# Kernel optimization log

Measured on AMD Instinct MI355X. Metric: run time of the kernel, lower is better.

Reference implementation:

```python
import jax, jax.numpy as jnp
import numpy as np
from math import log2

B, N, H, DH, BSZ = 4, 4096, 16, 64, 16
DIM = H * DH
EPS = 1e-8


def setup_inputs() -> dict:
    key = jax.random.key(0)
    ks = jax.random.split(key, 7)
    s = 0.02
    return {
        "hidden_states": jax.random.normal(ks[0], (B, N, DIM), jnp.float32),
        "Wq": jax.random.normal(ks[1], (DIM, DIM), jnp.float32) * s,
        "bq": jax.random.normal(ks[2], (DIM,), jnp.float32) * s,
        "Wk": jax.random.normal(ks[3], (DIM, DIM), jnp.float32) * s,
        "bk": jax.random.normal(ks[4], (DIM,), jnp.float32) * s,
        "Wv": jax.random.normal(ks[5], (DIM, DIM), jnp.float32) * s,
        "bv": jax.random.normal(ks[6], (DIM,), jnp.float32) * s,
    }


def _hattention(q, k, v):
    # q, k, v: [(b*h), n, dh]; n is a power of two divisible by BSZ
    bh, n, dh = q.shape
    num_levels = int(log2(n // BSZ)) - 2  # coarsen until 4 blocks remain

    # coarsening: mean-pool q and k, sum-pool v (mask=None path)
    qkvs = [(q, k, v)]
    for _ in range(num_levels):
        q = q.reshape(bh, -1, 2, dh).mean(axis=2)
        k = k.reshape(bh, -1, 2, dh).mean(axis=2)
        v = v.reshape(bh, -1, 2, dh).sum(axis=2)
        qkvs.append((q, k, v))

    def flip_blocks(t):
        # swap adjacent blocks to capture off-diagonal interactions
        nb = t.shape[1]
        return t.reshape(bh, nb // 2, 2, BSZ, dh)[:, :, ::-1].reshape(bh, nb, BSZ, dh)

    Ys = []
    L = len(qkvs)
    for ind in range(L):
        qq, kk, vv = qkvs[L - 1 - ind]  # reversed: coarsest first
        is_last = ind == L - 1          # finest level: pure block-diagonal
        blk = lambda t: t.reshape(bh, -1, BSZ, dh)
        qq, kk, vv = blk(qq), blk(kk), blk(vv)
        if not is_last:
            kk = flip_blocks(kk)
            vv = flip_blocks(vv)
        S = jnp.einsum('bnid,bnjd->bnij', qq, kk)
        S = S - jnp.max(S, axis=-1, keepdims=True)
        A = jnp.exp(S)  # unnormalized attention weights
        y = jnp.einsum('bnij,bnjd->bnid', A, vv)
        Ys.append((y.reshape(bh, -1, dh), A.sum(axis=-1).reshape(bh, -1)))

    # interpolate: upsample coarse numerators/denominators and accumulate
    Y, A = Ys[0]
    for Y_l, A_l in Ys[1:]:
        Y = jnp.repeat(Y, 2, axis=1) + Y_l
        A = jnp.repeat(A, 2, axis=1) + A_l
    return Y / (A + EPS)[..., None]


def reference(hidden_states, Wq, bq, Wk, bk, Wv, bv):
    b, n, d = hidden_states.shape
    q = hidden_states @ Wq + bq
    k = hidden_states @ Wk + bk
    v = hidden_states @ Wv + bv
    split_heads = lambda t: t.reshape(b, n, H, DH).transpose(0, 2, 1, 3).reshape(b * H, n, DH)
    q, k, v = split_heads(q), split_heads(k), split_heads(v)
    q = q * (DH ** -0.5)
    out = _hattention(q, k, v)  # [(b*h), n, dh]
    return out.reshape(b, H, n, DH).transpose(0, 2, 1, 3).reshape(b, n, H * DH)
```

## Files before the change

kernel.cpp:

```cpp
#include <hip/hip_runtime.h>
#include <hip/hip_bf16.h>

typedef unsigned short u16;
typedef unsigned int u32;
typedef __bf16 bf16x8 __attribute__((ext_vector_type(8)));
typedef float f32x4 __attribute__((ext_vector_type(4)));
typedef u16 u16x4 __attribute__((ext_vector_type(4)));
typedef u16 u16x8 __attribute__((ext_vector_type(8)));

#define N_    4096
#define H_    16
#define BH_   64
#define DIM_  1024
#define MTOK  16384

#define RB1 262144
#define RB2 393216
#define RB3 458752
#define RB4 491520
#define RB5 507904
#define RB6 516096

__device__ __forceinline__ float bf2f(u16 u) {
  union { u32 i; float f; } x; x.i = ((u32)u) << 16; return x.f;
}
__device__ __forceinline__ u16 f2bf(float f) {
  union { float f; u32 i; } x; x.f = f;
  u32 r = x.i + 0x7fffu + ((x.i >> 16) & 1u);
  return (u16)(r >> 16);
}

__device__ __forceinline__ void gload_lds16(const u16* g, u16* l) {
  __builtin_amdgcn_global_load_lds(
      (const __attribute__((address_space(1))) void*)g,
      (__attribute__((address_space(3))) void*)l, 16, 0, 0);
}

__global__ __launch_bounds__(256) void k_hid2bf(const float* __restrict__ in,
                                                u16* __restrict__ out, int n4) {
  int i = blockIdx.x * 256 + threadIdx.x;
  if (i >= n4) return;
  f32x4 v = reinterpret_cast<const f32x4*>(in)[i];
  u16x4 o;
  o[0] = f2bf(v[0]); o[1] = f2bf(v[1]); o[2] = f2bf(v[2]); o[3] = f2bf(v[3]);
  reinterpret_cast<u16x4*>(out)[i] = o;
}

__global__ __launch_bounds__(256) void k_transpose(const float* __restrict__ Wq,
                                                   const float* __restrict__ Wk,
                                                   const float* __restrict__ Wv,
                                                   u16* __restrict__ Wt) {
  __shared__ float tile[32][33];
  const float* W = (blockIdx.z == 0) ? Wq : ((blockIdx.z == 1) ? Wk : Wv);
  int n0 = blockIdx.x * 32, k0 = blockIdx.y * 32;
  int tx = threadIdx.x, ty = threadIdx.y;
  #pragma unroll
  for (int r = ty; r < 32; r += 8)
    tile[r][tx] = W[(size_t)(k0 + r) * DIM_ + n0 + tx];
  __syncthreads();
  u16* o = Wt + (size_t)blockIdx.z * DIM_ * DIM_;
  #pragma unroll
  for (int r = ty; r < 32; r += 8)
    o[(size_t)(n0 + r) * DIM_ + k0 + tx] = f2bf(tile[tx][r]);
}

__global__ __launch_bounds__(256) void k_qkv_gemm(
    const u16* __restrict__ hid,
    const u16* __restrict__ Wt,
    const float* __restrict__ bq, const float* __restrict__ bk, const float* __restrict__ bv,
    u16* __restrict__ qout, u16* __restrict__ kout, u16* __restrict__ vout) {
  const int wsel = blockIdx.z;
  const int m0 = blockIdx.x * 128;
  const int n0 = blockIdx.y * 128;
  __shared__ u16 As[128 * 64];
  __shared__ u16 Bs[128 * 64];
  const int t = threadIdx.x;
  const int lane = t & 63, wave = t >> 6;
  const int wm = (wave >> 1) * 64, wn = (wave & 1) * 64;
  f32x4 acc[4][4];
  #pragma unroll
  for (int m = 0; m < 4; m++)
    #pragma unroll
    for (int n = 0; n < 4; n++) acc[m][n] = (f32x4){0.f, 0.f, 0.f, 0.f};

  const int srow = t >> 3;
  const int sslot = (t & 7) ^ (srow & 7);
  const u16* Ag = hid + ((size_t)m0 + srow) * DIM_ + sslot * 8;
  const u16* Bg = Wt + (size_t)wsel * DIM_ * DIM_ + ((size_t)n0 + srow) * DIM_ + sslot * 8;
  u16* AsT = &As[t * 8];
  u16* BsT = &Bs[t * 8];
  const int lr = lane & 15, kg = lane >> 4;

  for (int k0 = 0; k0 < DIM_; k0 += 64) {
    #pragma unroll
    for (int j = 0; j < 4; j++) {
      gload_lds16(Ag + k0 + j * (32 * DIM_), AsT + j * 2048);
      gload_lds16(Bg + k0 + j * (32 * DIM_), BsT + j * 2048);
    }
    __syncthreads();
    #pragma unroll
    for (int ks = 0; ks < 2; ks++) {
      bf16x8 af[4], bfr[4];
      const int sw = ((ks * 4 + kg) ^ (lr & 7)) * 8;
      #pragma unroll
      for (int m = 0; m < 4; m++)
        af[m] = *reinterpret_cast<const bf16x8*>(&As[(wm + m * 16 + lr) * 64 + sw]);
      #pragma unroll
      for (int n = 0; n < 4; n++)
        bfr[n] = *reinterpret_cast<const bf16x8*>(&Bs[(wn + n * 16 + lr) * 64 + sw]);
      #pragma unroll
      for (int m = 0; m < 4; m++)
        #pragma unroll
        for (int n = 0; n < 4; n++)
          acc[m][n] = __builtin_amdgcn_mfma_f32_16x16x32_bf16(af[m], bfr[n], acc[m][n], 0, 0, 0);
    }
    __syncthreads();
  }

  const float* bias = (wsel == 0) ? bq : ((wsel == 1) ? bk : bv);
  u16* dst = (wsel == 0) ? qout : ((wsel == 1) ? kout : vout);
  const float scale = (wsel == 0) ? 0.125f : 1.0f;
  const bool isv = (wsel == 2);
  const float s1 = isv ? 1.f : 0.5f, s2 = isv ? 1.f : 0.25f;
  const float s3 = isv ? 1.f : 0.125f, s4 = isv ? 1.f : 0.0625f;
  const int rg = lane >> 4;
  const int b = m0 >> 12;
  const int posb = m0 & (N_ - 1);
  const int h = (n0 + wn) >> 6;
  const size_t bh = (size_t)(b * H_ + h);

  #pragma unroll
  for (int m = 0; m < 4; m++) {
    const int plm = wm + m * 16;
    #pragma unroll
    for (int n = 0; n < 4; n++) {
      const int d = n * 16 + lr;
      const float bias_v = bias[n0 + wn + d];
      float v0 = (acc[m][n][0] + bias_v) * scale;
      float v1 = (acc[m][n][1] + bias_v) * scale;
      float v2 = (acc[m][n][2] + bias_v) * scale;
      float v3 = (acc[m][n][3] + bias_v) * scale;
      const int pl = plm + rg * 4;
      size_t r0 = (bh * N_ + posb + pl) * 64 + d;
      dst[r0] = f2bf(v0); dst[r0 + 64] = f2bf(v1);
      dst[r0 + 128] = f2bf(v2); dst[r0 + 192] = f2bf(v3);
      float c1a = v0 + v1, c1b = v2 + v3;
      size_t r1 = ((size_t)RB1 + bh * 2048 + (size_t)((posb + pl) >> 1)) * 64 + d;
      dst[r1] = f2bf(c1a * s1);
      dst[r1 + 64] = f2bf(c1b * s1);
      float c2 = c1a + c1b;
      dst[((size_t)RB2 + bh * 1024 + (size_t)((posb + pl) >> 2)) * 64 + d] = f2bf(c2 * s2);
      float c3 = c2 + __shfl_xor(c2, 16);
      float c4 = c3 + __shfl_xor(c3, 32);
      if ((rg & 1) == 0)
        dst[((size_t)RB3 + bh * 512 + (size_t)(((posb + plm) >> 3) + (rg >> 1))) * 64 + d] =
            f2bf(c3 * s3);
      if (rg == 0)
        dst[((size_t)RB4 + bh * 256 + (size_t)((posb + plm) >> 4)) * 64 + d] = f2bf(c4 * s4);
    }
  }
}

__global__ __launch_bounds__(256) void k_coarsen56(u16* __restrict__ qb, u16* __restrict__ kb,
                                                   u16* __restrict__ vb) {
  int t = blockIdx.x * 256 + threadIdx.x;
  int dg = t & 7;
  int p6 = (t >> 3) & 63;
  int bh = (t >> 9) & 63;
  int z = t >> 15;
  u16* buf = (z == 0) ? qb : ((z == 1) ? kb : vb);
  const bool isv = (z == 2);
  const float s5 = isv ? 1.f : 0.5f, s6 = isv ? 1.f : 0.25f;
  const u16* src = buf + ((size_t)RB4 + bh * 256 + p6 * 4) * 64 + dg * 8;
  float a5[8], a6[8];
  #pragma unroll
  for (int e = 0; e < 8; e++) { a5[e] = 0.f; a6[e] = 0.f; }
  #pragma unroll
  for (int i = 0; i < 4; i++) {
    u16x8 x = *reinterpret_cast<const u16x8*>(src + (size_t)i * 64);
    #pragma unroll
    for (int e = 0; e < 8; e++) a5[e] += bf2f(x[e]);
    if ((i & 1) == 1) {
      u16x8 o;
      #pragma unroll
      for (int e = 0; e < 8; e++) { o[e] = f2bf(a5[e] * s5); a6[e] += a5[e]; a5[e] = 0.f; }
      *reinterpret_cast<u16x8*>(buf + ((size_t)RB5 + bh * 128 + p6 * 2 + (i >> 1)) * 64 + dg * 8) = o;
    }
  }
  u16x8 o;
  #pragma unroll
  for (int e = 0; e < 8; e++) o[e] = f2bf(a6[e] * s6);
  *reinterpret_cast<u16x8*>(buf + ((size_t)RB6 + bh * 64 + p6) * 64 + dg * 8) = o;
}

__device__ __forceinline__ void qk_softmax(const u16* __restrict__ qb_, size_t qrow,
                                           const u16* __restrict__ kb_, size_t kvrow,
                                           int lane, f32x4& p, float& asum) {
  const int lr = lane & 15, g = lane >> 4;
  const u16* kp = kb_ + (kvrow + lr) * 64 + g * 8;
  const u16* qp = qb_ + (qrow + lr) * 64 + g * 8;
  bf16x8 ka0 = *reinterpret_cast<const bf16x8*>(kp);
  bf16x8 ka1 = *reinterpret_cast<const bf16x8*>(kp + 32);
  bf16x8 qa0 = *reinterpret_cast<const bf16x8*>(qp);
  bf16x8 qa1 = *reinterpret_cast<const bf16x8*>(qp + 32);
  f32x4 s = (f32x4){0.f, 0.f, 0.f, 0.f};
  s = __builtin_amdgcn_mfma_f32_16x16x32_bf16(ka0, qa0, s, 0, 0, 0);
  s = __builtin_amdgcn_mfma_f32_16x16x32_bf16(ka1, qa1, s, 0, 0, 0);
  float mx = fmaxf(fmaxf(s[0], s[1]), fmaxf(s[2], s[3]));
  mx = fmaxf(mx, __shfl_xor(mx, 16));
  mx = fmaxf(mx, __shfl_xor(mx, 32));
  #pragma unroll
  for (int i = 0; i < 4; i++) p[i] = __expf(s[i] - mx);
  asum = p[0] + p[1] + p[2] + p[3];
  asum += __shfl_xor(asum, 16);
  asum += __shfl_xor(asum, 32);
}

__device__ __forceinline__ bf16x8 prep_pb(const f32x4& p, int lane) {
  const int g = lane >> 4;
  const int src = (lane & 15) + ((g & 1) << 5);
  float tl[4], th[4];
  #pragma unroll
  for (int i = 0; i < 4; i++) {
    tl[i] = __shfl(p[i], src);
    th[i] = __shfl(p[i], src + 16);
  }
  const bool act = (g < 2);
  union { u16 u[8]; bf16x8 b; } cvt;
  #pragma unroll
  for (int i = 0; i < 4; i++) {
    cvt.u[i] = act ? f2bf(tl[i]) : (u16)0;
    cvt.u[4 + i] = act ? f2bf(th[i]) : (u16)0;
  }
  return cvt.b;
}

__device__ __forceinline__ f32x4 pv_chunk(const u16* __restrict__ vb_, size_t kvrow,
                                          int c, int lane, bf16x8 pb) {
  const int lr = lane & 15, g = lane >> 4;
  const u16* vp = vb_ + (kvrow + (size_t)(g & 1) * 8) * 64 + c * 16 + lr;
  union { u16 u[8]; bf16x8 b; } va;
  #pragma unroll
  for (int e = 0; e < 8; e++) va.u[e] = vp[(size_t)e * 64];
  f32x4 y = (f32x4){0.f, 0.f, 0.f, 0.f};
  return __builtin_amdgcn_mfma_f32_16x16x32_bf16(va.b, pb, y, 0, 0, 0);
}

__global__ __launch_bounds__(256) void k_attn_rest(
    const u16* __restrict__ qb, const u16* __restrict__ kb, const u16* __restrict__ vb,
    u16* __restrict__ Yb, float* __restrict__ Ab) {
  const int wid = blockIdx.x * 4 + (threadIdx.x >> 6);
  const int lane = threadIdx.x & 63;
  const int rb = wid * 16;
  int r = rb, lnl = 11;
  while (r >= (64 << lnl)) { r -= (64 << lnl); --lnl; }
  const int posl = r & ((1 << lnl) - 1);
  const size_t qrow = (size_t)RB1 + rb;
  const size_t kvrow = qrow - posl + ((size_t)((((posl >> 4) ^ 1)) & ((1 << (lnl - 4)) - 1)) << 4);

  f32x4 p; float asum;
  qk_softmax(qb, qrow, kb, kvrow, lane, p, asum);
  if (lane < 16) Ab[rb + lane] = asum;
  bf16x8 pb = prep_pb(p, lane);

  const int lr = lane & 15, g = lane >> 4;
  #pragma unroll
  for (int c = 0; c < 4; c++) {
    f32x4 y = pv_chunk(vb, kvrow, c, lane, pb);
    u16x4 o;
    #pragma unroll
    for (int i = 0; i < 4; i++) o[i] = f2bf(y[i]);
    *reinterpret_cast<u16x4*>(Yb + (size_t)(rb + lr) * 64 + c * 16 + g * 4) = o;
  }
}

__global__ __launch_bounds__(256) void k_attn0(
    const u16* __restrict__ qb, const u16* __restrict__ kb, const u16* __restrict__ vb,
    const u16* __restrict__ Yb, const float* __restrict__ Ab, float* __restrict__ out) {
  const int wid = blockIdx.x * 4 + (threadIdx.x >> 6);
  const int lane = threadIdx.x & 63;
  const int rb = wid * 16;
  const int bh = rb >> 12, posb = rb & 4095;
  const size_t qrow = (size_t)rb, kvrow = (size_t)rb;

  f32x4 p; float asum;
  qk_softmax(qb, qrow, kb, kvrow, lane, p, asum);
  bf16x8 pb = prep_pb(p, lane);

  const int lr = lane & 15, g = lane >> 4;
  const int pos = posb + lr;
  float den = asum + 1e-8f;
  int ybase[6];
  #pragma unroll
  for (int l = 1; l <= 6; l++) {
    int st = 262144 - (262144 >> (l - 1));
    int idx = st + (bh << (12 - l)) + (pos >> l);
    den += Ab[idx];
    ybase[l - 1] = idx;
  }
  const float inv = 1.0f / den;

  const int b = bh >> 4, h = bh & 15;
  float* op = out + ((size_t)(b * N_ + pos)) * DIM_ + h * 64;
  #pragma unroll
  for (int c = 0; c < 4; c++) {
    f32x4 y = pv_chunk(vb, kvrow, c, lane, pb);
    #pragma unroll
    for (int l = 0; l < 6; l++) {
      u16x4 cy = *reinterpret_cast<const u16x4*>(Yb + (size_t)ybase[l] * 64 + c * 16 + g * 4);
      #pragma unroll
      for (int i = 0; i < 4; i++) y[i] += bf2f(cy[i]);
    }
    f32x4 w;
    #pragma unroll
    for (int i = 0; i < 4; i++) w[i] = y[i] * inv;
    *reinterpret_cast<f32x4*>(op + c * 16 + g * 4) = w;
  }
}

extern "C" void kernel_launch(void* const* d_in, const int* in_sizes, int n_in,
                              void* d_out, int out_size, void* d_ws, size_t ws_size,
                              hipStream_t stream) {
  const float* hid = (const float*)d_in[0];
  const float* Wq = (const float*)d_in[1];
  const float* bq = (const float*)d_in[2];
  const float* Wk = (const float*)d_in[3];
  const float* bk = (const float*)d_in[4];
  const float* Wv = (const float*)d_in[5];
  const float* bv = (const float*)d_in[6];
  float* out = (float*)d_out;
  char* ws = (char*)d_ws;

  u16* hidb = (u16*)(ws + 0);
  u16* Wt   = (u16*)(ws + 33554432);
  u16* Yb   = (u16*)(ws + 0);
  float* Ab = (float*)(ws + 33030144);
  u16* qb   = (u16*)(ws + 39845888);
  u16* kb   = (u16*)(ws + 106430464);
  u16* vb   = (u16*)(ws + 173015040);

  k_hid2bf<<<16384, 256, 0, stream>>>(hid, hidb, MTOK * DIM_ / 4);
  k_transpose<<<dim3(32, 32, 3), dim3(32, 8, 1), 0, stream>>>(Wq, Wk, Wv, Wt);
  k_qkv_gemm<<<dim3(128, 8, 3), 256, 0, stream>>>(hidb, Wt, bq, bk, bv, qb, kb, vb);
  k_coarsen56<<<384, 256, 0, stream>>>(qb, kb, vb);
  k_attn_rest<<<4032, 256, 0, stream>>>(qb, kb, vb, Yb, Ab);
  k_attn0<<<4096, 256, 0, stream>>>(qb, kb, vb, Yb, Ab, out);
}
```

Baseline: 240.5 us.

## Stage QKV GEMM epilogue through LDS for coalesced vector stores and coarsening

The GEMM epilogue now writes the biased, scaled bf16 tile into padded shared memory and then emits 16-byte vectorized global stores for the full-resolution output and for each coarsening level (1 through 4). Previously each lane wrote scattered 2-byte values, with shuffles used for the deeper levels. The change targets write coalescing. In exchange it enlarges shared memory, adds several barriers, and changes numerics because each coarse level is now built from bf16-rounded values of the previous level rather than fp32 sums.

```diff
diff --git a/kernel.cpp b/kernel.cpp
--- a/kernel.cpp
+++ b/kernel.cpp
@@ -20,6 +20,8 @@
 #define RB4 491520
 #define RB5 507904
 #define RB6 516096
+
+#define TS 136
 
 __device__ __forceinline__ float bf2f(u16 u) {
   union { u32 i; float f; } x; x.i = ((u32)u) << 16; return x.f;
@@ -72,8 +74,9 @@
   const int wsel = blockIdx.z;
   const int m0 = blockIdx.x * 128;
   const int n0 = blockIdx.y * 128;
-  __shared__ u16 As[128 * 64];
-  __shared__ u16 Bs[128 * 64];
+  __shared__ u16 smem[26112];
+  u16* As = smem;
+  u16* Bs = smem + 8192;
   const int t = threadIdx.x;
   const int lane = t & 63, wave = t >> 6;
   const int wm = (wave >> 1) * 64, wn = (wave & 1) * 64;
@@ -120,44 +123,103 @@
   const float* bias = (wsel == 0) ? bq : ((wsel == 1) ? bk : bv);
   u16* dst = (wsel == 0) ? qout : ((wsel == 1) ? kout : vout);
   const float scale = (wsel == 0) ? 0.125f : 1.0f;
-  const bool isv = (wsel == 2);
-  const float s1 = isv ? 1.f : 0.5f, s2 = isv ? 1.f : 0.25f;
-  const float s3 = isv ? 1.f : 0.125f, s4 = isv ? 1.f : 0.0625f;
-  const int rg = lane >> 4;
+  const float tfac = (wsel == 2) ? 1.0f : 0.5f;
   const int b = m0 >> 12;
   const int posb = m0 & (N_ - 1);
-  const int h = (n0 + wn) >> 6;
-  const size_t bh = (size_t)(b * H_ + h);
+  const int bh_base = b * H_ + (n0 >> 6);
+  u16* tile0 = smem;
+  u16* tile1 = smem + 17408;
 
   #pragma unroll
   for (int m = 0; m < 4; m++) {
-    const int plm = wm + m * 16;
     #pragma unroll
     for (int n = 0; n < 4; n++) {
-      const int d = n * 16 + lr;
-      const float bias_v = bias[n0 + wn + d];
-      float v0 = (acc[m][n][0] + bias_v) * scale;
-      float v1 = (acc[m][n][1] + bias_v) * scale;
-      float v2 = (acc[m][n][2] + bias_v) * scale;
-      float v3 = (acc[m][n][3] + bias_v) * scale;
-      const int pl = plm + rg * 4;
-      size_t r0 = (bh * N_ + posb + pl) * 64 + d;
-      dst[r0] = f2bf(v0); dst[r0 + 64] = f2bf(v1);
-      dst[r0 + 128] = f2bf(v2); dst[r0 + 192] = f2bf(v3);
-      float c1a = v0 + v1, c1b = v2 + v3;
-      size_t r1 = ((size_t)RB1 + bh * 2048 + (size_t)((posb + pl) >> 1)) * 64 + d;
-      dst[r1] = f2bf(c1a * s1);
-      dst[r1 + 64] = f2bf(c1b * s1);
-      float c2 = c1a + c1b;
-      dst[((size_t)RB2 + bh * 1024 + (size_t)((posb + pl) >> 2)) * 64 + d] = f2bf(c2 * s2);
-      float c3 = c2 + __shfl_xor(c2, 16);
-      float c4 = c3 + __shfl_xor(c3, 32);
-      if ((rg & 1) == 0)
-        dst[((size_t)RB3 + bh * 512 + (size_t)(((posb + plm) >> 3) + (rg >> 1))) * 64 + d] =
-            f2bf(c3 * s3);
-      if (rg == 0)
-        dst[((size_t)RB4 + bh * 256 + (size_t)((posb + plm) >> 4)) * 64 + d] = f2bf(c4 * s4);
-    }
+      const int col = wn + n * 16 + lr;
+      const float bias_v = bias[n0 + col];
+      #pragma unroll
+      for (int i = 0; i < 4; i++) {
+        const int row = wm + m * 16 + kg * 4 + i;
+        tile0[row * TS + col] = f2bf((acc[m][n][i] + bias_v) * scale);
+      }
+    }
+  }
+  __syncthreads();
+
+  {
+    const int r = t >> 1, hh = t & 1;
+    u16* gp = dst + ((size_t)(bh_base + hh) * N_ + posb + r) * 64;
+    const u16* lp = &tile0[r * TS + hh * 64];
+    #pragma unroll
+    for (int k = 0; k < 8; k++)
+      *reinterpret_cast<u16x8*>(gp + k * 8) = *reinterpret_cast<const u16x8*>(lp + k * 8);
+  }
+
+  {
+    const int j = t >> 2, q = t & 3;
+    const u16* pa = &tile0[(2 * j) * TS + q * 32];
+    const u16* pb = &tile0[(2 * j + 1) * TS + q * 32];
+    u16* tp = &tile1[j * TS + q * 32];
+    u16* gp = dst + ((size_t)RB1 + (size_t)(bh_base + (q >> 1)) * 2048 + (posb >> 1) + j) * 64 +
+              (q & 1) * 32;
+    #pragma unroll
+    for (int k = 0; k < 4; k++) {
+      u16x8 a = *reinterpret_cast<const u16x8*>(pa + k * 8);
+      u16x8 c = *reinterpret_cast<const u16x8*>(pb + k * 8);
+      u16x8 o;
+      #pragma unroll
+      for (int e = 0; e < 8; e++) o[e] = f2bf((bf2f(a[e]) + bf2f(c[e])) * tfac);
+      *reinterpret_cast<u16x8*>(tp + k * 8) = o;
+      *reinterpret_cast<u16x8*>(gp + k * 8) = o;
+    }
+  }
+  __syncthreads();
+
+  {
+    const int j = t >> 3, q = t & 7;
+    const u16* pa = &tile1[(2 * j) * TS + q * 16];
+    const u16* pb = &tile1[(2 * j + 1) * TS + q * 16];
+    u16* tp = &tile0[j * TS + q * 16];
+    u16* gp = dst + ((size_t)RB2 + (size_t)(bh_base + (q >> 2)) * 1024 + (posb >> 2) + j) * 64 +
+              (q & 3) * 16;
+    #pragma unroll
+    for (int k = 0; k < 2; k++) {
+      u16x8 a = *reinterpret_cast<const u16x8*>(pa + k * 8);
+      u16x8 c = *reinterpret_cast<const u16x8*>(pb + k * 8);
+      u16x8 o;
+      #pragma unroll
+      for (int e = 0; e < 8; e++) o[e] = f2bf((bf2f(a[e]) + bf2f(c[e])) * tfac);
+      *reinterpret_cast<u16x8*>(tp + k * 8) = o;
+      *reinterpret_cast<u16x8*>(gp + k * 8) = o;
+    }
+  }
+  __syncthreads();
+
+  {
+    const int j = t >> 4, q = t & 15;
+    const u16* pa = &tile0[(2 * j) * TS + q * 8];
+    const u16* pb = &tile0[(2 * j + 1) * TS + q * 8];
+    u16x8 a = *reinterpret_cast<const u16x8*>(pa);
+    u16x8 c = *reinterpret_cast<const u16x8*>(pb);
+    u16x8 o;
+    #pragma unroll
+    for (int e = 0; e < 8; e++) o[e] = f2bf((bf2f(a[e]) + bf2f(c[e])) * tfac);
+    *reinterpret_cast<u16x8*>(&tile1[j * TS + q * 8]) = o;
+    u16* gp = dst + ((size_t)RB3 + (size_t)(bh_base + (q >> 3)) * 512 + (posb >> 3) + j) * 64 +
+              (q & 7) * 8;
+    *reinterpret_cast<u16x8*>(gp) = o;
+  }
+  __syncthreads();
+
+  if (t < 128) {
+    const int j = t >> 4, q = t & 15;
+    u16x8 a = *reinterpret_cast<const u16x8*>(&tile1[(2 * j) * TS + q * 8]);
+    u16x8 c = *reinterpret_cast<const u16x8*>(&tile1[(2 * j + 1) * TS + q * 8]);
+    u16x8 o;
+    #pragma unroll
+    for (int e = 0; e < 8; e++) o[e] = f2bf((bf2f(a[e]) + bf2f(c[e])) * tfac);
+    u16* gp = dst + ((size_t)RB4 + (size_t)(bh_base + (q >> 3)) * 256 + (posb >> 4) + j) * 64 +
+              (q & 7) * 8;
+    *reinterpret_cast<u16x8*>(gp) = o;
   }
 }
 
```

Result: slower. 254.0 us (+5.6%).

## Fuse Q/K/V projections into one GEMM block sharing the A tile

Applied to the files above, without the earlier changes.

Each GEMM block now computes the Q, K and V outputs for its tile together. It loads the hidden-state A tile once and three B tiles per k-step, rather than launching three separate grids that each reload A. This cuts global and LDS traffic for the activations. The cost is three times the accumulator registers (192 floats per lane) and 64KB of LDS, which lowers occupancy and leaves 1024 blocks instead of 3072 to fill the CUs.

```diff
diff --git a/kernel.cpp b/kernel.cpp
--- a/kernel.cpp
+++ b/kernel.cpp
@@ -64,65 +64,68 @@
     o[(size_t)(n0 + r) * DIM_ + k0 + tx] = f2bf(tile[tx][r]);
 }
 
-__global__ __launch_bounds__(256) void k_qkv_gemm(
+__global__ __launch_bounds__(256, 2) void k_qkv_gemm(
     const u16* __restrict__ hid,
     const u16* __restrict__ Wt,
     const float* __restrict__ bq, const float* __restrict__ bk, const float* __restrict__ bv,
     u16* __restrict__ qout, u16* __restrict__ kout, u16* __restrict__ vout) {
-  const int wsel = blockIdx.z;
   const int m0 = blockIdx.x * 128;
   const int n0 = blockIdx.y * 128;
   __shared__ u16 As[128 * 64];
-  __shared__ u16 Bs[128 * 64];
+  __shared__ u16 Bs[3][128 * 64];
   const int t = threadIdx.x;
   const int lane = t & 63, wave = t >> 6;
   const int wm = (wave >> 1) * 64, wn = (wave & 1) * 64;
-  f32x4 acc[4][4];
-  #pragma unroll
-  for (int m = 0; m < 4; m++)
-    #pragma unroll
-    for (int n = 0; n < 4; n++) acc[m][n] = (f32x4){0.f, 0.f, 0.f, 0.f};
+  f32x4 acc[3][4][4];
+  #pragma unroll
+  for (int z = 0; z < 3; z++)
+    #pragma unroll
+    for (int m = 0; m < 4; m++)
+      #pragma unroll
+      for (int n = 0; n < 4; n++) acc[z][m][n] = (f32x4){0.f, 0.f, 0.f, 0.f};
 
   const int srow = t >> 3;
   const int sslot = (t & 7) ^ (srow & 7);
   const u16* Ag = hid + ((size_t)m0 + srow) * DIM_ + sslot * 8;
-  const u16* Bg = Wt + (size_t)wsel * DIM_ * DIM_ + ((size_t)n0 + srow) * DIM_ + sslot * 8;
+  const u16* Bg = Wt + ((size_t)n0 + srow) * DIM_ + sslot * 8;
   u16* AsT = &As[t * 8];
-  u16* BsT = &Bs[t * 8];
   const int lr = lane & 15, kg = lane >> 4;
 
   for (int k0 = 0; k0 < DIM_; k0 += 64) {
     #pragma unroll
-    for (int j = 0; j < 4; j++) {
+    for (int j = 0; j < 4; j++)
       gload_lds16(Ag + k0 + j * (32 * DIM_), AsT + j * 2048);
-      gload_lds16(Bg + k0 + j * (32 * DIM_), BsT + j * 2048);
+    #pragma unroll
+    for (int z = 0; z < 3; z++)
+      #pragma unroll
+      for (int j = 0; j < 4; j++)
+        gload_lds16(Bg + (size_t)z * DIM_ * DIM_ + k0 + j * (32 * DIM_),
+                    &Bs[z][t * 8 + j * 2048]);
+    __syncthreads();
+    #pragma unroll
+    for (int ks = 0; ks < 2; ks++) {
+      const int sw = ((ks * 4 + kg) ^ (lr & 7)) * 8;
+      bf16x8 af[4];
+      #pragma unroll
+      for (int m = 0; m < 4; m++)
+        af[m] = *reinterpret_cast<const bf16x8*>(&As[(wm + m * 16 + lr) * 64 + sw]);
+      #pragma unroll
+      for (int z = 0; z < 3; z++) {
+        bf16x8 bfr[4];
+        #pragma unroll
+        for (int n = 0; n < 4; n++)
+          bfr[n] = *reinterpret_cast<const bf16x8*>(&Bs[z][(wn + n * 16 + lr) * 64 + sw]);
+        #pragma unroll
+        for (int m = 0; m < 4; m++)
+          #pragma unroll
+          for (int n = 0; n < 4; n++)
+            acc[z][m][n] =
+                __builtin_amdgcn_mfma_f32_16x16x32_bf16(af[m], bfr[n], acc[z][m][n], 0, 0, 0);
+      }
     }
     __syncthreads();
-    #pragma unroll
-    for (int ks = 0; ks < 2; ks++) {
-      bf16x8 af[4], bfr[4];
-      const int sw = ((ks * 4 + kg) ^ (lr & 7)) * 8;
-      #pragma unroll
-      for (int m = 0; m < 4; m++)
-        af[m] = *reinterpret_cast<const bf16x8*>(&As[(wm + m * 16 + lr) * 64 + sw]);
-      #pragma unroll
-      for (int n = 0; n < 4; n++)
-        bfr[n] = *reinterpret_cast<const bf16x8*>(&Bs[(wn + n * 16 + lr) * 64 + sw]);
-      #pragma unroll
-      for (int m = 0; m < 4; m++)
-        #pragma unroll
-        for (int n = 0; n < 4; n++)
-          acc[m][n] = __builtin_amdgcn_mfma_f32_16x16x32_bf16(af[m], bfr[n], acc[m][n], 0, 0, 0);
-    }
-    __syncthreads();
-  }
-
-  const float* bias = (wsel == 0) ? bq : ((wsel == 1) ? bk : bv);
-  u16* dst = (wsel == 0) ? qout : ((wsel == 1) ? kout : vout);
-  const float scale = (wsel == 0) ? 0.125f : 1.0f;
-  const bool isv = (wsel == 2);
-  const float s1 = isv ? 1.f : 0.5f, s2 = isv ? 1.f : 0.25f;
-  const float s3 = isv ? 1.f : 0.125f, s4 = isv ? 1.f : 0.0625f;
+  }
+
   const int rg = lane >> 4;
   const int b = m0 >> 12;
   const int posb = m0 & (N_ - 1);
@@ -130,33 +133,42 @@
   const size_t bh = (size_t)(b * H_ + h);
 
   #pragma unroll
-  for (int m = 0; m < 4; m++) {
-    const int plm = wm + m * 16;
-    #pragma unroll
-    for (int n = 0; n < 4; n++) {
-      const int d = n * 16 + lr;
-      const float bias_v = bias[n0 + wn + d];
-      float v0 = (acc[m][n][0] + bias_v) * scale;
-      float v1 = (acc[m][n][1] + bias_v) * scale;
-      float v2 = (acc[m][n][2] + bias_v) * scale;
-      float v3 = (acc[m][n][3] + bias_v) * scale;
-      const int pl = plm + rg * 4;
-      size_t r0 = (bh * N_ + posb + pl) * 64 + d;
-      dst[r0] = f2bf(v0); dst[r0 + 64] = f2bf(v1);
-      dst[r0 + 128] = f2bf(v2); dst[r0 + 192] = f2bf(v3);
-      float c1a = v0 + v1, c1b = v2 + v3;
-      size_t r1 = ((size_t)RB1 + bh * 2048 + (size_t)((posb + pl) >> 1)) * 64 + d;
-      dst[r1] = f2bf(c1a * s1);
-      dst[r1 + 64] = f2bf(c1b * s1);
-      float c2 = c1a + c1b;
-      dst[((size_t)RB2 + bh * 1024 + (size_t)((posb + pl) >> 2)) * 64 + d] = f2bf(c2 * s2);
-      float c3 = c2 + __shfl_xor(c2, 16);
-      float c4 = c3 + __shfl_xor(c3, 32);
-      if ((rg & 1) == 0)
-        dst[((size_t)RB3 + bh * 512 + (size_t)(((posb + plm) >> 3) + (rg >> 1))) * 64 + d] =
-            f2bf(c3 * s3);
-      if (rg == 0)
-        dst[((size_t)RB4 + bh * 256 + (size_t)((posb + plm) >> 4)) * 64 + d] = f2bf(c4 * s4);
+  for (int z = 0; z < 3; z++) {
+    const float* bias = (z == 0) ? bq : ((z == 1) ? bk : bv);
+    u16* dst = (z == 0) ? qout : ((z == 1) ? kout : vout);
+    const float scale = (z == 0) ? 0.125f : 1.0f;
+    const bool isv = (z == 2);
+    const float s1 = isv ? 1.f : 0.5f, s2 = isv ? 1.f : 0.25f;
+    const float s3 = isv ? 1.f : 0.125f, s4 = isv ? 1.f : 0.0625f;
+    #pragma unroll
+    for (int m = 0; m < 4; m++) {
+      const int plm = wm + m * 16;
+      #pragma unroll
+      for (int n = 0; n < 4; n++) {
+        const int d = n * 16 + lr;
+        const float bias_v = bias[n0 + wn + d];
+        float v0 = (acc[z][m][n][0] + bias_v) * scale;
+        float v1 = (acc[z][m][n][1] + bias_v) * scale;
+        float v2 = (acc[z][m][n][2] + bias_v) * scale;
+        float v3 = (acc[z][m][n][3] + bias_v) * scale;
+        const int pl = plm + rg * 4;
+        size_t r0 = (bh * N_ + posb + pl) * 64 + d;
+        dst[r0] = f2bf(v0); dst[r0 + 64] = f2bf(v1);
+        dst[r0 + 128] = f2bf(v2); dst[r0 + 192] = f2bf(v3);
+        float c1a = v0 + v1, c1b = v2 + v3;
+        size_t r1 = ((size_t)RB1 + bh * 2048 + (size_t)((posb + pl) >> 1)) * 64 + d;
+        dst[r1] = f2bf(c1a * s1);
+        dst[r1 + 64] = f2bf(c1b * s1);
+        float c2 = c1a + c1b;
+        dst[((size_t)RB2 + bh * 1024 + (size_t)((posb + pl) >> 2)) * 64 + d] = f2bf(c2 * s2);
+        float c3 = c2 + __shfl_xor(c2, 16);
+        float c4 = c3 + __shfl_xor(c3, 32);
+        if ((rg & 1) == 0)
+          dst[((size_t)RB3 + bh * 512 + (size_t)(((posb + plm) >> 3) + (rg >> 1))) * 64 + d] =
+              f2bf(c3 * s3);
+        if (rg == 0)
+          dst[((size_t)RB4 + bh * 256 + (size_t)((posb + plm) >> 4)) * 64 + d] = f2bf(c4 * s4);
+      }
     }
   }
 }
@@ -341,7 +353,7 @@
 
   k_hid2bf<<<16384, 256, 0, stream>>>(hid, hidb, MTOK * DIM_ / 4);
   k_transpose<<<dim3(32, 32, 3), dim3(32, 8, 1), 0, stream>>>(Wq, Wk, Wv, Wt);
-  k_qkv_gemm<<<dim3(128, 8, 3), 256, 0, stream>>>(hidb, Wt, bq, bk, bv, qb, kb, vb);
+  k_qkv_gemm<<<dim3(128, 8, 1), 256, 0, stream>>>(hidb, Wt, bq, bk, bv, qb, kb, vb);
   k_coarsen56<<<384, 256, 0, stream>>>(qb, kb, vb);
   k_attn_rest<<<4032, 256, 0, stream>>>(qb, kb, vb, Yb, Ab);
   k_attn0<<<4096, 256, 0, stream>>>(qb, kb, vb, Yb, Ab, out);
```

After: 216.4 us. 1.11x faster.
